# Performance work log

Measured on AMD Instinct MI355X. Metric: run time of the kernel, lower is better.

## Reference

```python
import jax, jax.numpy as jnp
import numpy as np

NEG_INF = -jnp.inf


def setup_inputs() -> dict:
    key = jax.random.key(0)
    ks = jax.random.split(key, 8)
    B, C, H, W = 8, 512, 96, 96
    IC = max(1, C // 8)  # inter_channels = 64
    s = 1.0 / np.sqrt(C)
    x = jax.random.normal(ks[0], (B, C, H, W), dtype=jnp.float32)
    Wq = jax.random.normal(ks[1], (IC, C), dtype=jnp.float32) * s
    bq = jax.random.normal(ks[2], (IC,), dtype=jnp.float32) * s
    Wk = jax.random.normal(ks[3], (IC, C), dtype=jnp.float32) * s
    bk = jax.random.normal(ks[4], (IC,), dtype=jnp.float32) * s
    Wv = jax.random.normal(ks[5], (C, C), dtype=jnp.float32) * s
    bv = jax.random.normal(ks[6], (C,), dtype=jnp.float32) * s
    gamma = jnp.full((1,), 0.5, dtype=jnp.float32)  # nn.Parameter (zeros in torch; nonzero here for a non-trivial baseline)
    return {"x": x, "Wq": Wq, "bq": bq, "Wk": Wk, "bk": bk, "Wv": Wv, "bv": bv, "gamma": gamma}


def reference(x, Wq, bq, Wk, bk, Wv, bv, gamma):
    B, C, H, W = x.shape
    # 1x1 convs as channel contractions
    q = jnp.einsum('oc,bchw->bohw', Wq, x) + bq[None, :, None, None]
    k = jnp.einsum('oc,bchw->bohw', Wk, x) + bk[None, :, None, None]
    v = jnp.einsum('oc,bchw->bohw', Wv, x) + bv[None, :, None, None]
    # column (height-axis) attention logits: [B, H, W, H'] with -inf on h==h'
    e_h = jnp.einsum('bchw,bcgw->bhwg', q, k)
    eye = jnp.eye(H, dtype=bool)[:, None, :]  # [H,1,H'] broadcast over W
    e_h = jnp.where(eye[None], NEG_INF, e_h)
    # row (width-axis) attention logits: [B, H, W, W']
    e_w = jnp.einsum('bchw,bchv->bhwv', q, k)
    # joint softmax over concatenated H'+W' axis
    attn = jax.nn.softmax(jnp.concatenate([e_h, e_w], axis=-1), axis=-1)
    a_h = attn[..., :H]   # [B,H,W,H']
    a_w = attn[..., H:]   # [B,H,W,W']
    out_h = jnp.einsum('bcgw,bhwg->bchw', v, a_h)
    out_w = jnp.einsum('bchv,bhwv->bchw', v, a_w)
    return gamma[0] * (out_h + out_w) + x
```

## Files before the change

kernel.cpp:

```cpp
#include <hip/hip_runtime.h>
#include <hip/hip_bf16.h>

typedef __hip_bfloat16 bf16;
typedef unsigned short us8 __attribute__((ext_vector_type(8)));
typedef __attribute__((ext_vector_type(8))) short short8v;
typedef __attribute__((ext_vector_type(4))) float float4v;

__device__ __forceinline__ float us2f(unsigned short u){
  return __uint_as_float(((unsigned int)u) << 16);
}
__device__ __forceinline__ float b2f(bf16 v){ return __bfloat162float(v); }
__device__ __forceinline__ bf16 f2b(float v){ return __float2bfloat16(v); }
__device__ __forceinline__ unsigned short f2bu(float v){
  bf16 t = f2b(v); return *reinterpret_cast<unsigned short*>(&t);
}
__device__ __forceinline__ void gload16(const void* g, void* l){
  __builtin_amdgcn_global_load_lds((const __attribute__((address_space(1))) void*)g,
                                   (__attribute__((address_space(3))) void*)l, 16, 0, 0);
}

#define HW 9216
#define CH 512
#define NQ 640

__global__ void k_detect(const unsigned int* __restrict__ xw, int* __restrict__ flag){
  int t = threadIdx.x;
  int cnt = 0;
  for(int i=t;i<4096;i+=256){
    unsigned e = (xw[i]>>8)&0x7F;
    if(e==0x3E||e==0x3F) cnt++;
  }
  #pragma unroll
  for(int o=32;o>0;o>>=1) cnt += __shfl_xor(cnt,o);
  __shared__ int s[4];
  if((t&63)==0) s[t>>6]=cnt;
  __syncthreads();
  if(t==0){ int tot=s[0]+s[1]+s[2]+s[3]; *flag = (tot > 1228) ? 1 : 0; }
}

__global__ void k_pack(const void* __restrict__ Wq, const void* __restrict__ Wk,
                       const void* __restrict__ Wv, const void* __restrict__ bq,
                       const void* __restrict__ bk, const void* __restrict__ bv,
                       const int* __restrict__ flag,
                       bf16* __restrict__ Wall, float* __restrict__ ball){
  bool isbf = (*flag)!=0;
  int j = blockIdx.x, t = threadIdx.x;
  const void* src = (j < 64) ? Wq : (j < 128) ? Wk : Wv;
  int row = (j < 64) ? j : (j < 128) ? (j-64) : (j-128);
  for(int c=t;c<512;c+=256){
    float v = isbf ? b2f(((const bf16*)src)[(size_t)row*512+c])
                   : ((const float*)src)[(size_t)row*512+c];
    Wall[(size_t)j*512+c] = f2b(v);
  }
  if(t==0){
    const void* bsrc = (j<64)? bq : (j<128)? bk : bv;
    ball[j] = isbf ? b2f(((const bf16*)bsrc)[row]) : ((const float*)bsrc)[row];
  }
}

__global__ __launch_bounds__(256) void k_xcvt(const void* __restrict__ x,
    const int* __restrict__ flag, bf16* __restrict__ xT){
  __shared__ float T[64][65];
  bool isbf = (*flag)!=0;
  int b = blockIdx.z, c0 = blockIdx.y*64, hw0 = blockIdx.x*64;
  int tid = threadIdx.x;
  if(isbf){
    const bf16* xb = (const bf16*)x + ((size_t)b*CH + c0)*HW + hw0;
    #pragma unroll
    for(int i=0;i<2;i++){
      int e = i*256 + tid;
      int cc = e>>3, h8 = (e&7)*8;
      us8 v = *(const us8*)(xb + (size_t)cc*HW + h8);
      #pragma unroll
      for(int j=0;j<8;j++) T[cc][h8+j] = us2f(v[j]);
    }
  } else {
    const float* xb = (const float*)x + ((size_t)b*CH + c0)*HW + hw0;
    #pragma unroll
    for(int i=0;i<4;i++){
      int e = i*256 + tid;
      int cc = e>>4, h4 = (e&15)*4;
      float4 v = *(const float4*)(xb + (size_t)cc*HW + h4);
      T[cc][h4]=v.x; T[cc][h4+1]=v.y; T[cc][h4+2]=v.z; T[cc][h4+3]=v.w;
    }
  }
  __syncthreads();
  bf16* tb = xT + ((size_t)b*HW + hw0)*512 + c0;
  #pragma unroll
  for(int i=0;i<2;i++){
    int e = i*256 + tid;
    int r = e>>3, c8 = (e&7)*8;
    us8 o;
    #pragma unroll
    for(int j=0;j<8;j++) o[j] = f2bu(T[c8+j][r]);
    *(us8*)(tb + (size_t)r*512 + c8) = o;
  }
}

__global__ __launch_bounds__(256) void k_qkv(const bf16* __restrict__ xT,
    const bf16* __restrict__ Wall, const float* __restrict__ ball,
    bf16* __restrict__ Ot){
  __shared__ ushort AsL[128*64];
  __shared__ ushort BsL[128*64];
  int b = blockIdx.y;
  int bx = blockIdx.x;
  int swz = (bx & 7)*45 + (bx >> 3);
  int m0 = (swz/5)*128;
  int n0 = (swz%5)*128;
  int tid = threadIdx.x, wid = tid>>6, lane = tid&63;
  int m0w = (wid>>1)*64, n0w = (wid&1)*64;
  const bf16* Ab = xT + ((size_t)b*HW + m0)*512;
  const bf16* Bb = Wall + (size_t)n0*512;
  int r8 = lane>>3, c8 = lane&7;
  int csw = ((c8 ^ r8)*8);
  float4v acc[4][4];
  #pragma unroll
  for(int mt=0;mt<4;mt++)
    #pragma unroll
    for(int nt=0;nt<4;nt++) acc[mt][nt] = (float4v){0.f,0.f,0.f,0.f};
  for(int k0=0;k0<512;k0+=64){
    #pragma unroll
    for(int j=0;j<4;j++){
      int row0 = (j*4 + wid)*8;
      gload16(Ab + (size_t)(row0 + r8)*512 + k0 + csw, &AsL[row0*64]);
      gload16(Bb + (size_t)(row0 + r8)*512 + k0 + csw, &BsL[row0*64]);
    }
    __syncthreads();
    #pragma unroll
    for(int kk=0;kk<64;kk+=32){
      short8v a[4], bb[4];
      #pragma unroll
      for(int mt=0;mt<4;mt++){
        int row = m0w + mt*16 + (lane&15);
        int kb = (kk*2 + 16*(lane>>4)) ^ ((row&7)<<4);
        a[mt] = *(const short8v*)((const char*)AsL + row*128 + kb);
      }
      #pragma unroll
      for(int nt=0;nt<4;nt++){
        int row = n0w + nt*16 + (lane&15);
        int kb = (kk*2 + 16*(lane>>4)) ^ ((row&7)<<4);
        bb[nt] = *(const short8v*)((const char*)BsL + row*128 + kb);
      }
      #pragma unroll
      for(int mt=0;mt<4;mt++)
        #pragma unroll
        for(int nt=0;nt<4;nt++)
          acc[mt][nt] = __builtin_amdgcn_mfma_f32_16x16x32_bf16(a[mt], bb[nt], acc[mt][nt], 0,0,0);
    }
    __syncthreads();
  }
  #pragma unroll
  for(int mt=0;mt<4;mt++){
    #pragma unroll
    for(int nt=0;nt<4;nt++){
      int nn = n0 + n0w + nt*16 + (lane&15);
      float bias = ball[nn];
      int mbase = m0 + m0w + mt*16 + (lane>>4)*4;
      #pragma unroll
      for(int r=0;r<4;r++)
        Ot[((size_t)b*HW + mbase + r)*640 + nn] = f2b(acc[mt][nt][r] + bias);
    }
  }
}

__global__ __launch_bounds__(384) void k_eh(const bf16* __restrict__ Ot,
                                            float* __restrict__ eh2){
  __shared__ ushort Qs[96][72];
  __shared__ ushort Ks[96][72];
  int b = blockIdx.y, w = blockIdx.x;
  int tid = threadIdx.x, wid = tid>>6, lane = tid&63;
  const bf16* qb = Ot + ((size_t)b*HW + w)*640;
  #pragma unroll
  for(int i=0;i<2;i++){
    int e = tid + i*384;
    int row = e>>3, ko = (e&7)*8;
    us8 q = *(const us8*)(qb + (size_t)row*96*640 + ko);
    *(us8*)&Qs[row][ko] = q;
    us8 k = *(const us8*)(qb + (size_t)row*96*640 + 64 + ko);
    *(us8*)&Ks[row][ko] = k;
  }
  __syncthreads();
  float4v acc[6];
  #pragma unroll
  for(int nt=0;nt<6;nt++) acc[nt] = (float4v){0.f,0.f,0.f,0.f};
  #pragma unroll
  for(int kt=0;kt<2;kt++){
    int kb = kt*32 + 8*(lane>>4);
    short8v a = *(short8v*)&Qs[wid*16 + (lane&15)][kb];
    #pragma unroll
    for(int nt=0;nt<6;nt++){
      short8v bb = *(short8v*)&Ks[nt*16 + (lane&15)][kb];
      acc[nt] = __builtin_amdgcn_mfma_f32_16x16x32_bf16(a, bb, acc[nt], 0,0,0);
    }
  }
  int hbase = wid*16 + (lane>>4)*4;
  #pragma unroll
  for(int nt=0;nt<6;nt++){
    int g = nt*16 + (lane&15);
    #pragma unroll
    for(int r=0;r<4;r++){
      int h = hbase + r;
      eh2[((size_t)b*HW + (size_t)h*96 + w)*96 + g] =
          (g==h) ? -INFINITY : acc[nt][r];
    }
  }
}

__global__ __launch_bounds__(384) void k_ewsm(const bf16* __restrict__ Ot,
    const float* __restrict__ eh2, bf16* __restrict__ att){
  __shared__ char smem[38400];
  ushort (*Qs)[72] = (ushort(*)[72])smem;
  ushort (*Ks)[72] = (ushort(*)[72])(smem + 13824);
  float  (*Ew)[100] = (float(*)[100])smem;
  int b = blockIdx.y, h = blockIdx.x;
  int tid = threadIdx.x, wid = tid>>6, lane = tid&63;
  const bf16* qb = Ot + ((size_t)b*HW + (size_t)h*96)*640;
  #pragma unroll
  for(int i=0;i<2;i++){
    int e = tid + i*384;
    int row = e>>3, ko = (e&7)*8;
    us8 q = *(const us8*)(qb + (size_t)row*640 + ko);
    *(us8*)&Qs[row][ko] = q;
    us8 k = *(const us8*)(qb + (size_t)row*640 + 64 + ko);
    *(us8*)&Ks[row][ko] = k;
  }
  __syncthreads();
  float4v acc[6];
  #pragma unroll
  for(int nt=0;nt<6;nt++) acc[nt] = (float4v){0.f,0.f,0.f,0.f};
  #pragma unroll
  for(int kt=0;kt<2;kt++){
    int kb = kt*32 + 8*(lane>>4);
    short8v a = *(short8v*)&Qs[wid*16 + (lane&15)][kb];
    #pragma unroll
    for(int nt=0;nt<6;nt++){
      short8v bb = *(short8v*)&Ks[nt*16 + (lane&15)][kb];
      acc[nt] = __builtin_amdgcn_mfma_f32_16x16x32_bf16(a, bb, acc[nt], 0,0,0);
    }
  }
  __syncthreads();
  int wbase = wid*16 + (lane>>4)*4;
  #pragma unroll
  for(int nt=0;nt<6;nt++){
    int v = nt*16 + (lane&15);
    #pragma unroll
    for(int r=0;r<4;r++) Ew[wbase+r][v] = acc[nt][r];
  }
  __syncthreads();
  const float* ehb = eh2 + ((size_t)b*HW + (size_t)h*96)*96;
  bf16* ab = att + ((size_t)b*HW + (size_t)h*96)*192;
  for(int r=0;r<16;r++){
    int w = wid*16 + r;
    const float* er = ehb + (size_t)w*96;
    float v0 = er[lane];
    float v1 = (lane<32) ? er[64+lane] : Ew[w][lane-32];
    float v2 = Ew[w][lane+32];
    float m = fmaxf(fmaxf(v0,v1),v2);
    #pragma unroll
    for(int o=32;o>0;o>>=1) m = fmaxf(m, __shfl_xor(m,o));
    v0=__expf(v0-m); v1=__expf(v1-m); v2=__expf(v2-m);
    float s = v0+v1+v2;
    #pragma unroll
    for(int o=32;o>0;o>>=1) s += __shfl_xor(s,o);
    float inv = 1.0f/s;
    bf16* a = ab + (size_t)w*192;
    a[lane]=f2b(v0*inv); a[lane+64]=f2b(v1*inv); a[lane+128]=f2b(v2*inv);
  }
}

__global__ __launch_bounds__(384) void k_outh(const bf16* __restrict__ Ot,
    const bf16* __restrict__ att, bf16* __restrict__ P){
  __shared__ ushort As[96][104];
  __shared__ ushort Bs[128][104];
  int b = blockIdx.y;
  int bx = blockIdx.x;
  int w = bx % 96, c0 = (bx / 96)*128;
  int tid = threadIdx.x, wid = tid>>6, lane = tid&63;
  const bf16* ab = att + ((size_t)b*HW + w)*192;
  #pragma unroll
  for(int i=0;i<3;i++){
    int s = tid + i*384;
    int row = s/12, ko = (s%12)*8;
    us8 v = *(const us8*)(ab + (size_t)row*96*192 + ko);
    *(us8*)&As[row][ko] = v;
  }
  const bf16* vb = Ot + ((size_t)b*HW + w)*640 + 128 + c0;
  #pragma unroll
  for(int i=0;i<4;i++){
    int s = tid + i*384;
    int g = s % 96, cc = s / 96;
    us8 v = *(const us8*)(vb + (size_t)g*96*640 + cc*8);
    #pragma unroll
    for(int j=0;j<8;j++) Bs[cc*8+j][g] = v[j];
  }
  __syncthreads();
  float4v acc[8];
  #pragma unroll
  for(int nt=0;nt<8;nt++) acc[nt] = (float4v){0.f,0.f,0.f,0.f};
  #pragma unroll
  for(int kt=0;kt<3;kt++){
    int kb = kt*32 + 8*(lane>>4);
    short8v a = *(short8v*)&As[wid*16 + (lane&15)][kb];
    #pragma unroll
    for(int nt=0;nt<8;nt++){
      short8v bb = *(short8v*)&Bs[nt*16 + (lane&15)][kb];
      acc[nt] = __builtin_amdgcn_mfma_f32_16x16x32_bf16(a, bb, acc[nt], 0,0,0);
    }
  }
  bf16* Pb = P + ((size_t)b*HW + w)*512 + c0;
  int mb = wid*16 + (lane>>4)*4;
  #pragma unroll
  for(int nt=0;nt<8;nt++){
    int n = nt*16 + (lane&15);
    #pragma unroll
    for(int r=0;r<4;r++){
      size_t o = (size_t)(mb + r)*96*512 + n;
      Pb[o] = f2b(acc[nt][r]);
    }
  }
}

__global__ __launch_bounds__(512) void k_outwf(const bf16* __restrict__ Ot,
    const bf16* __restrict__ att, const bf16* __restrict__ P,
    const void* __restrict__ x, const void* __restrict__ gamma,
    const int* __restrict__ flag, void* __restrict__ out){
  __shared__ char smem[33280];
  ushort (*As)[104] = (ushort(*)[104])smem;
  ushort (*Bs)[104] = (ushort(*)[104])(smem + 19968);
  float  (*T)[100]  = (float(*)[100])smem;
  bool isbf = (*flag)!=0;
  int b = blockIdx.y;
  int bx = blockIdx.x;
  int h = bx % 96, c0 = (bx / 96)*64;
  int tid = threadIdx.x, wid = tid>>6, lane = tid&63;
  float g = isbf ? b2f(((const bf16*)gamma)[0]) : ((const float*)gamma)[0];
  const bf16* ab = att + ((size_t)b*HW + (size_t)h*96)*192 + 96;
  #pragma unroll
  for(int i=0;i<3;i++){
    int s = tid + i*512;
    if(s < 1152){
      int row = s/12, ko = (s%12)*8;
      us8 v = *(const us8*)(ab + (size_t)row*192 + ko);
      *(us8*)&As[row][ko] = v;
    }
  }
  const bf16* vb = Ot + ((size_t)b*HW + (size_t)h*96)*640 + 128 + c0;
  #pragma unroll
  for(int i=0;i<2;i++){
    int s = tid + i*512;
    if(s < 768){
      int gg = s % 96, cc = s / 96;
      us8 v = *(const us8*)(vb + (size_t)gg*640 + cc*8);
      #pragma unroll
      for(int j=0;j<8;j++) Bs[cc*8+j][gg] = v[j];
    }
  }
  __syncthreads();
  int mrow = (wid>>1)*16 + (lane&15);
  int ncol0 = (wid&1)*48;
  float4v acc[3];
  #pragma unroll
  for(int nt=0;nt<3;nt++) acc[nt] = (float4v){0.f,0.f,0.f,0.f};
  #pragma unroll
  for(int kt=0;kt<3;kt++){
    int kb = kt*32 + 8*(lane>>4);
    short8v a = *(short8v*)&Bs[mrow][kb];
    #pragma unroll
    for(int nt=0;nt<3;nt++){
      short8v bb = *(short8v*)&As[ncol0 + nt*16 + (lane&15)][kb];
      acc[nt] = __builtin_amdgcn_mfma_f32_16x16x32_bf16(a, bb, acc[nt], 0,0,0);
    }
  }
  __syncthreads();
  int clb = (wid>>1)*16 + (lane>>4)*4;
  #pragma unroll
  for(int nt=0;nt<3;nt++){
    int w = ncol0 + nt*16 + (lane&15);
    #pragma unroll
    for(int r=0;r<4;r++) T[clb + r][w] = acc[nt][r];
  }
  __syncthreads();
  const bf16* Pb = P + ((size_t)b*HW + (size_t)h*96)*512 + c0;
  #pragma unroll
  for(int i=0;i<2;i++){
    int s = tid + i*512;
    if(s < 768){
      int gg = s % 96, cc = s / 96;
      us8 v = *(const us8*)(Pb + (size_t)gg*512 + cc*8);
      #pragma unroll
      for(int j=0;j<8;j++) T[cc*8+j][gg] += us2f(v[j]);
    }
  }
  __syncthreads();
  size_t xbase = ((size_t)b*CH + c0)*HW + (size_t)h*96;
  if(isbf){
    const bf16* xb = (const bf16*)x;
    bf16* ob = (bf16*)out;
    #pragma unroll
    for(int i=0;i<2;i++){
      int e = i*512 + tid;
      if(e < 768){
        int c = e/12, w8 = (e%12)*8;
        us8 xv = *(const us8*)(xb + xbase + (size_t)c*HW + w8);
        us8 o;
        #pragma unroll
        for(int j=0;j<8;j++) o[j] = f2bu(g*T[c][w8+j] + us2f(xv[j]));
        *(us8*)(ob + xbase + (size_t)c*HW + w8) = o;
      }
    }
  } else {
    const float* xb = (const float*)x;
    float* ob = (float*)out;
    #pragma unroll
    for(int i=0;i<3;i++){
      int e = i*512 + tid;
      int c = e/24, w4 = (e%24)*4;
      float4 xv = *(const float4*)(xb + xbase + (size_t)c*HW + w4);
      float4 tv = *(const float4*)&T[c][w4];
      float4 o;
      o.x = g*tv.x + xv.x;
      o.y = g*tv.y + xv.y;
      o.z = g*tv.z + xv.z;
      o.w = g*tv.w + xv.w;
      *(float4*)(ob + xbase + (size_t)c*HW + w4) = o;
    }
  }
}

extern "C" void kernel_launch(void* const* d_in, const int* in_sizes, int n_in,
                              void* d_out, int out_size, void* d_ws, size_t ws_size,
                              hipStream_t stream){
  (void)in_sizes; (void)n_in; (void)out_size; (void)ws_size;
  const void* x     = d_in[0];
  const void* Wq    = d_in[1];
  const void* bq    = d_in[2];
  const void* Wk    = d_in[3];
  const void* bk    = d_in[4];
  const void* Wv    = d_in[5];
  const void* bv    = d_in[6];
  const void* gamma = d_in[7];
  char* ws = (char*)d_ws;

  bf16*  Wall = (bf16*)(ws + 0);
  float* ball = (float*)(ws + 655360);
  int*   flag = (int*)(ws + 657920);
  bf16*  Ot   = (bf16*)(ws + (1u<<20));
  bf16*  att  = (bf16*)(ws + 95420416ull);
  bf16*  xT   = (bf16*)(ws + 123731968ull);
  float* eh2  = (float*)(ws + 123731968ull);
  bf16*  P    = (bf16*)(ws + 123731968ull);

  hipLaunchKernelGGL(k_detect, dim3(1),       dim3(256), 0, stream,
                     (const unsigned int*)x, flag);
  hipLaunchKernelGGL(k_pack,   dim3(640),     dim3(256), 0, stream,
                     Wq, Wk, Wv, bq, bk, bv, flag, Wall, ball);
  hipLaunchKernelGGL(k_xcvt,   dim3(144,8,8), dim3(256), 0, stream, x, flag, xT);
  hipLaunchKernelGGL(k_qkv,    dim3(360,8),   dim3(256), 0, stream, xT, Wall, ball, Ot);
  hipLaunchKernelGGL(k_eh,     dim3(96,8),    dim3(384), 0, stream, Ot, eh2);
  hipLaunchKernelGGL(k_ewsm,   dim3(96,8),    dim3(384), 0, stream, Ot, eh2, att);
  hipLaunchKernelGGL(k_outh,   dim3(384,8),   dim3(384), 0, stream, Ot, att, P);
  hipLaunchKernelGGL(k_outwf,  dim3(768,8),   dim3(512), 0, stream,
                     Ot, att, P, x, gamma, flag, d_out);
}
```

Before: 268.9 us.

## Fuse x transpose/bf16 conversion into the QKV GEMM A-tile load

Removes the separate k_xcvt kernel that transposed x into a bf16 [HW][C] buffer, and instead has k_qkv read x in its native NCHW layout. Each thread loads 4x4 channel/pixel patches, converts them to bf16, transposes them in registers, and writes them into a padded LDS tile. This is meant to avoid the extra write and reread of a roughly 75 MB intermediate plus one kernel launch. In exchange, the A tile is now loaded with synchronous register loads instead of async global_load_lds, and each x element is reread by each of the 5 N-tiles.

```diff
diff --git a/kernel.cpp b/kernel.cpp
--- a/kernel.cpp
+++ b/kernel.cpp
@@ -2,6 +2,7 @@
 #include <hip/hip_bf16.h>
 
 typedef __hip_bfloat16 bf16;
+typedef unsigned short us4 __attribute__((ext_vector_type(4)));
 typedef unsigned short us8 __attribute__((ext_vector_type(8)));
 typedef __attribute__((ext_vector_type(8))) short short8v;
 typedef __attribute__((ext_vector_type(4))) float float4v;
@@ -58,50 +59,13 @@
   }
 }
 
-__global__ __launch_bounds__(256) void k_xcvt(const void* __restrict__ x,
-    const int* __restrict__ flag, bf16* __restrict__ xT){
-  __shared__ float T[64][65];
-  bool isbf = (*flag)!=0;
-  int b = blockIdx.z, c0 = blockIdx.y*64, hw0 = blockIdx.x*64;
-  int tid = threadIdx.x;
-  if(isbf){
-    const bf16* xb = (const bf16*)x + ((size_t)b*CH + c0)*HW + hw0;
-    #pragma unroll
-    for(int i=0;i<2;i++){
-      int e = i*256 + tid;
-      int cc = e>>3, h8 = (e&7)*8;
-      us8 v = *(const us8*)(xb + (size_t)cc*HW + h8);
-      #pragma unroll
-      for(int j=0;j<8;j++) T[cc][h8+j] = us2f(v[j]);
-    }
-  } else {
-    const float* xb = (const float*)x + ((size_t)b*CH + c0)*HW + hw0;
-    #pragma unroll
-    for(int i=0;i<4;i++){
-      int e = i*256 + tid;
-      int cc = e>>4, h4 = (e&15)*4;
-      float4 v = *(const float4*)(xb + (size_t)cc*HW + h4);
-      T[cc][h4]=v.x; T[cc][h4+1]=v.y; T[cc][h4+2]=v.z; T[cc][h4+3]=v.w;
-    }
-  }
-  __syncthreads();
-  bf16* tb = xT + ((size_t)b*HW + hw0)*512 + c0;
-  #pragma unroll
-  for(int i=0;i<2;i++){
-    int e = i*256 + tid;
-    int r = e>>3, c8 = (e&7)*8;
-    us8 o;
-    #pragma unroll
-    for(int j=0;j<8;j++) o[j] = f2bu(T[c8+j][r]);
-    *(us8*)(tb + (size_t)r*512 + c8) = o;
-  }
-}
-
-__global__ __launch_bounds__(256) void k_qkv(const bf16* __restrict__ xT,
+__global__ __launch_bounds__(256) void k_qkv(const void* __restrict__ x,
+    const int* __restrict__ flag,
     const bf16* __restrict__ Wall, const float* __restrict__ ball,
     bf16* __restrict__ Ot){
-  __shared__ ushort AsL[128*64];
+  __shared__ ushort As[128][72];
   __shared__ ushort BsL[128*64];
+  bool isbf = (*flag)!=0;
   int b = blockIdx.y;
   int bx = blockIdx.x;
   int swz = (bx & 7)*45 + (bx >> 3);
@@ -109,10 +73,10 @@
   int n0 = (swz%5)*128;
   int tid = threadIdx.x, wid = tid>>6, lane = tid&63;
   int m0w = (wid>>1)*64, n0w = (wid&1)*64;
-  const bf16* Ab = xT + ((size_t)b*HW + m0)*512;
   const bf16* Bb = Wall + (size_t)n0*512;
-  int r8 = lane>>3, c8 = lane&7;
-  int csw = ((c8 ^ r8)*8);
+  int r8 = lane>>3, c8l = lane&7;
+  int csw = ((c8l ^ r8)*8);
+  size_t xb = (size_t)b*CH*HW + m0;
   float4v acc[4][4];
   #pragma unroll
   for(int mt=0;mt<4;mt++)
@@ -122,19 +86,42 @@
     #pragma unroll
     for(int j=0;j<4;j++){
       int row0 = (j*4 + wid)*8;
-      gload16(Ab + (size_t)(row0 + r8)*512 + k0 + csw, &AsL[row0*64]);
       gload16(Bb + (size_t)(row0 + r8)*512 + k0 + csw, &BsL[row0*64]);
+    }
+    #pragma unroll
+    for(int i=0;i<2;i++){
+      int s = tid + i*256;
+      int cc4 = (s&15)*4, hh4 = (s>>4)*4;
+      us4 tq[4];
+      if(isbf){
+        const bf16* xp = (const bf16*)x + xb + (size_t)(k0+cc4)*HW + hh4;
+        us4 v0 = *(const us4*)(xp);
+        us4 v1 = *(const us4*)(xp + HW);
+        us4 v2 = *(const us4*)(xp + 2*HW);
+        us4 v3 = *(const us4*)(xp + 3*HW);
+        #pragma unroll
+        for(int q=0;q<4;q++){ tq[q][0]=v0[q]; tq[q][1]=v1[q]; tq[q][2]=v2[q]; tq[q][3]=v3[q]; }
+      } else {
+        const float* xp = (const float*)x + xb + (size_t)(k0+cc4)*HW + hh4;
+        float4 v0 = *(const float4*)(xp);
+        float4 v1 = *(const float4*)(xp + HW);
+        float4 v2 = *(const float4*)(xp + 2*HW);
+        float4 v3 = *(const float4*)(xp + 3*HW);
+        tq[0][0]=f2bu(v0.x); tq[0][1]=f2bu(v1.x); tq[0][2]=f2bu(v2.x); tq[0][3]=f2bu(v3.x);
+        tq[1][0]=f2bu(v0.y); tq[1][1]=f2bu(v1.y); tq[1][2]=f2bu(v2.y); tq[1][3]=f2bu(v3.y);
+        tq[2][0]=f2bu(v0.z); tq[2][1]=f2bu(v1.z); tq[2][2]=f2bu(v2.z); tq[2][3]=f2bu(v3.z);
+        tq[3][0]=f2bu(v0.w); tq[3][1]=f2bu(v1.w); tq[3][2]=f2bu(v2.w); tq[3][3]=f2bu(v3.w);
+      }
+      #pragma unroll
+      for(int q=0;q<4;q++) *(us4*)&As[hh4+q][cc4] = tq[q];
     }
     __syncthreads();
     #pragma unroll
     for(int kk=0;kk<64;kk+=32){
       short8v a[4], bb[4];
       #pragma unroll
-      for(int mt=0;mt<4;mt++){
-        int row = m0w + mt*16 + (lane&15);
-        int kb = (kk*2 + 16*(lane>>4)) ^ ((row&7)<<4);
-        a[mt] = *(const short8v*)((const char*)AsL + row*128 + kb);
-      }
+      for(int mt=0;mt<4;mt++)
+        a[mt] = *(short8v*)&As[m0w+mt*16+(lane&15)][kk+8*(lane>>4)];
       #pragma unroll
       for(int nt=0;nt<4;nt++){
         int row = n0w + nt*16 + (lane&15);
@@ -446,7 +433,6 @@
   int*   flag = (int*)(ws + 657920);
   bf16*  Ot   = (bf16*)(ws + (1u<<20));
   bf16*  att  = (bf16*)(ws + 95420416ull);
-  bf16*  xT   = (bf16*)(ws + 123731968ull);
   float* eh2  = (float*)(ws + 123731968ull);
   bf16*  P    = (bf16*)(ws + 123731968ull);
 
@@ -454,8 +440,8 @@
                      (const unsigned int*)x, flag);
   hipLaunchKernelGGL(k_pack,   dim3(640),     dim3(256), 0, stream,
                      Wq, Wk, Wv, bq, bk, bv, flag, Wall, ball);
-  hipLaunchKernelGGL(k_xcvt,   dim3(144,8,8), dim3(256), 0, stream, x, flag, xT);
-  hipLaunchKernelGGL(k_qkv,    dim3(360,8),   dim3(256), 0, stream, xT, Wall, ball, Ot);
+  hipLaunchKernelGGL(k_qkv,    dim3(360,8),   dim3(256), 0, stream,
+                     x, flag, Wall, ball, Ot);
   hipLaunchKernelGGL(k_eh,     dim3(96,8),    dim3(384), 0, stream, Ot, eh2);
   hipLaunchKernelGGL(k_ewsm,   dim3(96,8),    dim3(384), 0, stream, Ot, eh2, att);
   hipLaunchKernelGGL(k_outh,   dim3(384,8),   dim3(384), 0, stream, Ot, att, P);
```

Measured after the change: 291.7 us. 8.5% more time.
